# Performance work log

Hardware: AMD Instinct MI355X
Metric: run time of the kernel (lower is better)

## Reference

```python
import jax, jax.numpy as jnp
import numpy as np

B, EH, T = 8, 768, 512
PH, U = 320, 128
JH, C = 320, 34


def setup_inputs() -> dict:
    key = jax.random.key(0)
    ks = jax.random.split(key, 8)
    s_enc = 1.0 / np.sqrt(EH)
    s_pred = 1.0 / np.sqrt(PH)
    s_out = 1.0 / np.sqrt(JH)
    return {
        "enc": jax.random.normal(ks[0], (B, EH, T), dtype=jnp.float32),
        "dec": jax.random.normal(ks[1], (B, PH, U), dtype=jnp.float32),
        "W_enc": jax.random.normal(ks[2], (JH, EH), dtype=jnp.float32) * s_enc,
        "b_enc": jax.random.normal(ks[3], (JH,), dtype=jnp.float32) * s_enc,
        "W_pred": jax.random.normal(ks[4], (JH, PH), dtype=jnp.float32) * s_pred,
        "b_pred": jax.random.normal(ks[5], (JH,), dtype=jnp.float32) * s_pred,
        "W_out": jax.random.normal(ks[6], (C, JH), dtype=jnp.float32) * s_out,
        "b_out": jax.random.normal(ks[7], (C,), dtype=jnp.float32) * s_out,
    }


def reference(enc, dec, W_enc, b_enc, W_pred, b_pred, W_out, b_out):
    # enc: (B, EH, T) channels-first -> project each frame: (B, T, JH)
    e = jnp.einsum("bht,jh->btj", enc, W_enc) + b_enc
    # dec: (B, PH, U) -> (B, U, JH)
    p = jnp.einsum("bhu,ju->buj".replace("u,ju", "u,jh").replace("bhu", "bhu"), dec, W_pred) + b_pred if False else jnp.einsum("bhu,jh->buj", dec, W_pred) + b_pred
    # broadcast sum -> (B, T, U, JH), ReLU, small linear, log_softmax over classes
    h = jax.nn.relu(e[:, :, None, :] + p[:, None, :, :])
    logits = jnp.einsum("btuj,cj->btuc", h, W_out) + b_out
    return jax.nn.log_softmax(logits, axis=-1)
```

## Files before the change

kernel.cpp:

```cpp
#include <hip/hip_runtime.h>

#define B_ 8
#define EH_ 768
#define T_ 512
#define PH_ 320
#define U_ 128
#define JH_ 320
#define C_ 34
#define LDW 324
#define EOFF (66 * LDW)

typedef _Float16 f16x8 __attribute__((ext_vector_type(8)));
typedef _Float16 f16x4 __attribute__((ext_vector_type(4)));
typedef float f32x4 __attribute__((ext_vector_type(4)));
typedef f32x4 f32x4u __attribute__((aligned(8)));

static __device__ __forceinline__ f16x8 relu_sum8(f16x8 a, f16x8 b) {
    f16x8 s = a + b;
    f16x8 z = (f16x8)(_Float16)0.f;
    return __builtin_elementwise_max(s, z);
}

__global__ __launch_bounds__(256) void prep_kernel(
    const float* __restrict__ enc, const float* __restrict__ dec,
    const float* __restrict__ Wenc, const float* __restrict__ Wpred,
    const float* __restrict__ Wout,
    _Float16* __restrict__ enc_t, _Float16* __restrict__ dec_t,
    _Float16* __restrict__ wenc, _Float16* __restrict__ wpred,
    _Float16* __restrict__ wout)
{
    __shared__ _Float16 tile[32][36];
    const int NE = 16 * 24 * B_;
    const int ND = 4 * 10 * B_;
    const int tid = threadIdx.x;
    int bid = blockIdx.x;

    if (bid < NE + ND) {
        const float* src; _Float16* dst; int H, N, n0, h0, b;
        if (bid < NE) {
            src = enc; dst = enc_t; H = EH_; N = T_;
            n0 = (bid % 16) * 32; h0 = ((bid / 16) % 24) * 32; b = bid / (16 * 24);
        } else {
            int i = bid - NE;
            src = dec; dst = dec_t; H = PH_; N = U_;
            n0 = (i % 4) * 32; h0 = ((i / 4) % 10) * 32; b = i / 40;
        }
        const int tx = tid & 7, ty = tid >> 3;
        float4 v = *(const float4*)&src[((size_t)b * H + h0 + ty) * N + n0 + tx * 4];
        f16x4 t;
        t[0] = (_Float16)v.x; t[1] = (_Float16)v.y; t[2] = (_Float16)v.z; t[3] = (_Float16)v.w;
        *(f16x4*)&tile[ty][tx * 4] = t;
        __syncthreads();
        f16x4 o;
        o[0] = tile[tx * 4 + 0][ty];
        o[1] = tile[tx * 4 + 1][ty];
        o[2] = tile[tx * 4 + 2][ty];
        o[3] = tile[tx * 4 + 3][ty];
        *(f16x4*)&dst[((size_t)b * N + n0 + ty) * H + h0 + tx * 4] = o;
    } else {
        const int t1 = JH_ * EH_, t2 = JH_ * PH_, t3 = C_ * JH_;
        int i = (bid - NE - ND) * 256 + tid;
        if (i < t1)                wenc[i] = (_Float16)Wenc[i];
        else if (i < t1 + t2)      wpred[i - t1] = (_Float16)Wpred[i - t1];
        else if (i < t1 + t2 + t3) wout[i - t1 - t2] = (_Float16)Wout[i - t1 - t2];
    }
}

__global__ __launch_bounds__(256) void proj_kernel(
    const _Float16* __restrict__ enc_t, const _Float16* __restrict__ dec_t,
    const _Float16* __restrict__ wenc, const _Float16* __restrict__ wpred,
    const float* __restrict__ b_enc, const float* __restrict__ b_pred,
    _Float16* __restrict__ e_f, _Float16* __restrict__ p_f)
{
    const int tid = threadIdx.x;
    const int wave = tid >> 6, lane = tid & 63;
    const int lrow = lane & 15, quad = lane >> 4;

    int wid = blockIdx.x * 4 + wave;
    const int We = (T_ / 16) * (JH_ / 32) * B_;
    const _Float16 *src, *W; const float* bias; _Float16* dst; int H, N;
    if (wid < We) { src = enc_t; W = wenc;  bias = b_enc;  dst = e_f; H = EH_; N = T_; }
    else { wid -= We; src = dec_t; W = wpred; bias = b_pred; dst = p_f; H = PH_; N = U_; }

    const int njt = JH_ / 32;
    const int ntn = N / 16;
    const int jt = wid % njt; int r = wid / njt;
    const int nt = r % ntn; const int b = r / ntn;
    const int n0 = nt * 16, j0 = jt * 32;

    const _Float16* ap  = src + ((size_t)b * N + n0 + lrow) * H + quad * 8;
    const _Float16* wp0 = W + (size_t)(j0 + lrow) * H + quad * 8;
    const _Float16* wp1 = wp0 + (size_t)16 * H;

    f32x4 acc0 = {0.f, 0.f, 0.f, 0.f};
    f32x4 acc1 = {0.f, 0.f, 0.f, 0.f};
#pragma unroll 4
    for (int k = 0; k < H; k += 32) {
        f16x8 af = *(const f16x8*)(ap + k);
        f16x8 w0 = *(const f16x8*)(wp0 + k);
        f16x8 w1 = *(const f16x8*)(wp1 + k);
        acc0 = __builtin_amdgcn_mfma_f32_16x16x32_f16(w0, af, acc0, 0, 0, 0);
        acc1 = __builtin_amdgcn_mfma_f32_16x16x32_f16(w1, af, acc1, 0, 0, 0);
    }
    const float4 bj0 = *(const float4*)&bias[j0 + quad * 4];
    const float4 bj1 = *(const float4*)&bias[j0 + 16 + quad * 4];
    f16x4 o0, o1;
    o0[0] = (_Float16)(acc0[0] + bj0.x);
    o0[1] = (_Float16)(acc0[1] + bj0.y);
    o0[2] = (_Float16)(acc0[2] + bj0.z);
    o0[3] = (_Float16)(acc0[3] + bj0.w);
    o1[0] = (_Float16)(acc1[0] + bj1.x);
    o1[1] = (_Float16)(acc1[1] + bj1.y);
    o1[2] = (_Float16)(acc1[2] + bj1.z);
    o1[3] = (_Float16)(acc1[3] + bj1.w);
    _Float16* dp = dst + ((size_t)b * N + n0 + lrow) * JH_ + j0;
    *(f16x4*)&dp[quad * 4]      = o0;
    *(f16x4*)&dp[16 + quad * 4] = o1;
}

__global__ __launch_bounds__(256, 3) __attribute__((amdgpu_waves_per_eu(3)))
void joint_kernel(
    const _Float16* __restrict__ e_f, const _Float16* __restrict__ p_f,
    const _Float16* __restrict__ wout_f, const float* __restrict__ b_out,
    float* __restrict__ out)
{
    __shared__ alignas(16) _Float16 lds[66 * LDW + 16 * 320];

    const int tid = threadIdx.x;
    const int t0 = blockIdx.x * 16;
    const int u0 = blockIdx.y * 32;
    const int b  = blockIdx.z;

    {
        const uint4* sw = (const uint4*)wout_f;
        for (int i = tid; i < 34 * 40; i += 256) {
            int rr = i / 40, k8 = i % 40;
            *(uint4*)&lds[rr * LDW + k8 * 8] = sw[i];
        }
        const uint4* sp = (const uint4*)(p_f + ((size_t)b * U_ + u0) * JH_);
        for (int i = tid; i < 32 * 40; i += 256) {
            int rr = i / 40, k8 = i % 40;
            *(uint4*)&lds[(34 + rr) * LDW + k8 * 8] = sp[i];
        }
        const uint4* se = (const uint4*)(e_f + ((size_t)b * T_ + t0) * JH_);
        for (int i = tid; i < 16 * 40; i += 256) {
            int rr = i / 40, k8 = i % 40;
            *(uint4*)&lds[EOFF + rr * 320 + k8 * 8] = se[i];
        }
    }
    __syncthreads();

    const int lane = tid & 63, wave = tid >> 6;
    const int lrow = lane & 15, quad = lane >> 4;
    const int lk = quad * 8;
    const int urow0 = 34 + lrow;
    const int urow1 = 34 + 16 + lrow;
    const int tbase = wave * 4;

    f32x4 acc0[4][3], acc1[4][3];
#pragma unroll
    for (int tt = 0; tt < 4; ++tt)
#pragma unroll
        for (int c = 0; c < 3; ++c) {
            acc0[tt][c] = (f32x4){0.f, 0.f, 0.f, 0.f};
            acc1[tt][c] = (f32x4){0.f, 0.f, 0.f, 0.f};
        }

    for (int kk = 0; kk < 10; ++kk) {
        const int k = lk + kk * 32;
        f16x8 pv0 = *(const f16x8*)&lds[urow0 * LDW + k];
        f16x8 pv1 = *(const f16x8*)&lds[urow1 * LDW + k];
        f16x8 w0  = *(const f16x8*)&lds[(0  + lrow) * LDW + k];
        f16x8 w1  = *(const f16x8*)&lds[(16 + lrow) * LDW + k];
        f16x8 w2  = *(const f16x8*)&lds[(32 + lrow) * LDW + k];
#pragma unroll
        for (int tt = 0; tt < 4; ++tt) {
            f16x8 ev = *(const f16x8*)&lds[EOFF + (tbase + tt) * 320 + k];
            f16x8 h0 = relu_sum8(pv0, ev);
            f16x8 h1 = relu_sum8(pv1, ev);
            acc0[tt][0] = __builtin_amdgcn_mfma_f32_16x16x32_f16(w0, h0, acc0[tt][0], 0, 0, 0);
            acc0[tt][1] = __builtin_amdgcn_mfma_f32_16x16x32_f16(w1, h0, acc0[tt][1], 0, 0, 0);
            acc0[tt][2] = __builtin_amdgcn_mfma_f32_16x16x32_f16(w2, h0, acc0[tt][2], 0, 0, 0);
            acc1[tt][0] = __builtin_amdgcn_mfma_f32_16x16x32_f16(w0, h1, acc1[tt][0], 0, 0, 0);
            acc1[tt][1] = __builtin_amdgcn_mfma_f32_16x16x32_f16(w1, h1, acc1[tt][1], 0, 0, 0);
            acc1[tt][2] = __builtin_amdgcn_mfma_f32_16x16x32_f16(w2, h1, acc1[tt][2], 0, 0, 0);
        }
    }

    const f32x4 B0 = *(const f32x4*)&b_out[quad * 4];
    const f32x4 B1 = *(const f32x4*)&b_out[16 + quad * 4];
    const bool q0 = (quad == 0);
    const float b2x = q0 ? b_out[32] : 0.f;
    const float b2y = q0 ? b_out[33] : 0.f;

    float* pob = out + (((size_t)b * T_ + t0 + tbase) * U_ + u0 + lrow) * C_;
#pragma unroll
    for (int tt = 0; tt < 4; ++tt) {
        {
            const f32x4 a0 = acc0[tt][0] + B0;
            const f32x4 a1 = acc0[tt][1] + B1;
            const float v2x = acc0[tt][2][0] + b2x;
            const float v2y = acc0[tt][2][1] + b2y;
            float s = __expf(a0[0]) + __expf(a0[1]) + __expf(a0[2]) + __expf(a0[3])
                    + __expf(a1[0]) + __expf(a1[1]) + __expf(a1[2]) + __expf(a1[3]);
            if (q0) s += __expf(v2x) + __expf(v2y);
            s += __shfl_xor(s, 16);
            s += __shfl_xor(s, 32);
            const float lse = __logf(s);
            *(f32x4u*)&pob[quad * 4]      = a0 - lse;
            *(f32x4u*)&pob[16 + quad * 4] = a1 - lse;
            if (q0) *(float2*)&pob[32]    = make_float2(v2x - lse, v2y - lse);
        }
        {
            float* pb = pob + 16 * C_;
            const f32x4 a0 = acc1[tt][0] + B0;
            const f32x4 a1 = acc1[tt][1] + B1;
            const float v2x = acc1[tt][2][0] + b2x;
            const float v2y = acc1[tt][2][1] + b2y;
            float s = __expf(a0[0]) + __expf(a0[1]) + __expf(a0[2]) + __expf(a0[3])
                    + __expf(a1[0]) + __expf(a1[1]) + __expf(a1[2]) + __expf(a1[3]);
            if (q0) s += __expf(v2x) + __expf(v2y);
            s += __shfl_xor(s, 16);
            s += __shfl_xor(s, 32);
            const float lse = __logf(s);
            *(f32x4u*)&pb[quad * 4]      = a0 - lse;
            *(f32x4u*)&pb[16 + quad * 4] = a1 - lse;
            if (q0) *(float2*)&pb[32]    = make_float2(v2x - lse, v2y - lse);
        }
        pob += U_ * C_;
    }
}

extern "C" void kernel_launch(void* const* d_in, const int* in_sizes, int n_in,
                              void* d_out, int out_size, void* d_ws, size_t ws_size,
                              hipStream_t stream) {
    const float* enc    = (const float*)d_in[0];
    const float* dec    = (const float*)d_in[1];
    const float* W_enc  = (const float*)d_in[2];
    const float* b_enc  = (const float*)d_in[3];
    const float* W_pred = (const float*)d_in[4];
    const float* b_pred = (const float*)d_in[5];
    const float* W_out  = (const float*)d_in[6];
    const float* b_out  = (const float*)d_in[7];
    float* out = (float*)d_out;

    _Float16* enc_t  = (_Float16*)d_ws;
    _Float16* dec_t  = enc_t  + (size_t)B_ * T_ * EH_;
    _Float16* wenc_f = dec_t  + (size_t)B_ * U_ * PH_;
    _Float16* wpred_f= wenc_f + (size_t)JH_ * EH_;
    _Float16* wout_f = wpred_f+ (size_t)JH_ * PH_;
    _Float16* e_f    = wout_f + (size_t)C_ * JH_;
    _Float16* p_f    = e_f    + (size_t)B_ * T_ * JH_;

    const int NE = 16 * 24 * B_, ND = 4 * 10 * B_;
    const int NW = (JH_ * EH_ + JH_ * PH_ + C_ * JH_ + 255) / 256;
    prep_kernel<<<dim3(NE + ND + NW), 256, 0, stream>>>(
        enc, dec, W_enc, W_pred, W_out, enc_t, dec_t, wenc_f, wpred_f, wout_f);

    const int We = (T_ / 16) * (JH_ / 32) * B_;
    const int Wp = (U_ / 16) * (JH_ / 32) * B_;
    proj_kernel<<<dim3((We + Wp) / 4), 256, 0, stream>>>(
        enc_t, dec_t, wenc_f, wpred_f, b_enc, b_pred, e_f, p_f);

    joint_kernel<<<dim3(T_ / 16, U_ / 32, B_), 256, 0, stream>>>(e_f, p_f, wout_f, b_out, out);
}
```

Baseline: 150.8 us.

## Stage log-softmax output through LDS for coalesced 16-byte global stores

The epilogue now writes log-softmax results into shared memory tiles, one 16-row u-half at a time. After a barrier, all 256 threads copy each 16x16x34 float tile to global memory with contiguous float4 stores. The aim is to replace the scattered, partially aligned per-lane stores (34-float rows) with fully coalesced writes of the large output. In exchange it adds extra barriers, an LDS round trip, and index division in the copy loop.

```diff
diff --git a/kernel.cpp b/kernel.cpp
--- a/kernel.cpp
+++ b/kernel.cpp
@@ -13,7 +13,6 @@
 typedef _Float16 f16x8 __attribute__((ext_vector_type(8)));
 typedef _Float16 f16x4 __attribute__((ext_vector_type(4)));
 typedef float f32x4 __attribute__((ext_vector_type(4)));
-typedef f32x4 f32x4u __attribute__((aligned(8)));
 
 static __device__ __forceinline__ f16x8 relu_sum8(f16x8 a, f16x8 b) {
     f16x8 s = a + b;
@@ -186,6 +185,7 @@
             acc1[tt][2] = __builtin_amdgcn_mfma_f32_16x16x32_f16(w2, h1, acc1[tt][2], 0, 0, 0);
         }
     }
+    __syncthreads();
 
     const f32x4 B0 = *(const f32x4*)&b_out[quad * 4];
     const f32x4 B1 = *(const f32x4*)&b_out[16 + quad * 4];
@@ -193,41 +193,43 @@
     const float b2x = q0 ? b_out[32] : 0.f;
     const float b2y = q0 ? b_out[33] : 0.f;
 
-    float* pob = out + (((size_t)b * T_ + t0 + tbase) * U_ + u0 + lrow) * C_;
-#pragma unroll
-    for (int tt = 0; tt < 4; ++tt) {
-        {
-            const f32x4 a0 = acc0[tt][0] + B0;
-            const f32x4 a1 = acc0[tt][1] + B1;
-            const float v2x = acc0[tt][2][0] + b2x;
-            const float v2y = acc0[tt][2][1] + b2y;
-            float s = __expf(a0[0]) + __expf(a0[1]) + __expf(a0[2]) + __expf(a0[3])
-                    + __expf(a1[0]) + __expf(a1[1]) + __expf(a1[2]) + __expf(a1[3]);
+    float* ldsF = (float*)lds;
+
+#pragma unroll
+    for (int uh = 0; uh < 2; ++uh) {
+#pragma unroll
+        for (int tt = 0; tt < 4; ++tt) {
+            const f32x4 A0 = (uh ? acc1 : acc0)[tt][0] + B0;
+            const f32x4 A1 = (uh ? acc1 : acc0)[tt][1] + B1;
+            const float v2x = (uh ? acc1 : acc0)[tt][2][0] + b2x;
+            const float v2y = (uh ? acc1 : acc0)[tt][2][1] + b2y;
+
+            float s = __expf(A0[0]) + __expf(A0[1]) + __expf(A0[2]) + __expf(A0[3])
+                    + __expf(A1[0]) + __expf(A1[1]) + __expf(A1[2]) + __expf(A1[3]);
             if (q0) s += __expf(v2x) + __expf(v2y);
             s += __shfl_xor(s, 16);
             s += __shfl_xor(s, 32);
             const float lse = __logf(s);
-            *(f32x4u*)&pob[quad * 4]      = a0 - lse;
-            *(f32x4u*)&pob[16 + quad * 4] = a1 - lse;
-            if (q0) *(float2*)&pob[32]    = make_float2(v2x - lse, v2y - lse);
-        }
+
+            float* lp = ldsF + ((size_t)((tbase + tt) * 16 + lrow)) * C_;
+            *(float2*)&lp[quad * 4]          = make_float2(A0[0] - lse, A0[1] - lse);
+            *(float2*)&lp[quad * 4 + 2]      = make_float2(A0[2] - lse, A0[3] - lse);
+            *(float2*)&lp[16 + quad * 4]     = make_float2(A1[0] - lse, A1[1] - lse);
+            *(float2*)&lp[16 + quad * 4 + 2] = make_float2(A1[2] - lse, A1[3] - lse);
+            if (q0) *(float2*)&lp[32]        = make_float2(v2x - lse, v2y - lse);
+        }
+        __syncthreads();
         {
-            float* pb = pob + 16 * C_;
-            const f32x4 a0 = acc1[tt][0] + B0;
-            const f32x4 a1 = acc1[tt][1] + B1;
-            const float v2x = acc1[tt][2][0] + b2x;
-            const float v2y = acc1[tt][2][1] + b2y;
-            float s = __expf(a0[0]) + __expf(a0[1]) + __expf(a0[2]) + __expf(a0[3])
-                    + __expf(a1[0]) + __expf(a1[1]) + __expf(a1[2]) + __expf(a1[3]);
-            if (q0) s += __expf(v2x) + __expf(v2y);
-            s += __shfl_xor(s, 16);
-            s += __shfl_xor(s, 32);
-            const float lse = __logf(s);
-            *(f32x4u*)&pb[quad * 4]      = a0 - lse;
-            *(f32x4u*)&pb[16 + quad * 4] = a1 - lse;
-            if (q0) *(float2*)&pb[32]    = make_float2(v2x - lse, v2y - lse);
-        }
-        pob += U_ * C_;
+            float* gbase = out + (((size_t)b * T_ + t0) * U_ + u0 + uh * 16) * C_;
+            for (int i = tid; i < 16 * 16 * C_ / 4; i += 256) {
+                const int f  = i * 4;
+                const int tl = f / (16 * C_);
+                const int rem = f - tl * (16 * C_);
+                const f32x4 v = *(const f32x4*)&ldsF[f];
+                *(f32x4*)&gbase[(size_t)tl * (U_ * C_) + rem] = v;
+            }
+        }
+        if (uh == 0) __syncthreads();
     }
 }
 
```

Result: no change. 149.8 us (-0.7%).
